# Kernel tuning notes

Hardware: AMD Instinct MI355X
Metric: run time of the kernel (lower is better)

Reference implementation:

```python
import jax, jax.numpy as jnp
import numpy as np

N_NODES = 50000
IN_CH = 128
HID = 128
N_EDGES = 800000


def _glorot(key, shape):
    fan_in, fan_out = shape[0], shape[1]
    lim = (6.0 / (fan_in + fan_out)) ** 0.5
    return jax.random.uniform(key, shape, jnp.float32, -lim, lim)


def setup_inputs() -> dict:
    key = jax.random.key(0)
    ks = jax.random.split(key, 8)
    x = jax.random.normal(ks[0], (N_NODES, IN_CH), jnp.float32)
    edge_index = jax.random.randint(ks[1], (2, N_EDGES), 0, N_NODES, jnp.int64)
    return {
        "x": x,
        "edge_index": edge_index,
        # SAGEConv1: lin_l (with bias) applied to mean-aggregated neighbors,
        # lin_r (no bias) applied to root features (PyG defaults, mean aggr)
        "W1l": _glorot(ks[2], (IN_CH, HID)),
        "b1l": jnp.zeros((HID,), jnp.float32),
        "W1r": _glorot(ks[3], (IN_CH, HID)),
        # SAGEConv2
        "W2l": _glorot(ks[4], (HID, HID)),
        "b2l": jnp.zeros((HID,), jnp.float32),
        "W2r": _glorot(ks[5], (HID, HID)),
        # final Linear(hidden, 1)
        "Wout": _glorot(ks[6], (HID, 1)),
        "bout": jnp.zeros((1,), jnp.float32),
    }


def _sage_conv(x, src, dst, Wl, bl, Wr, n_nodes):
    # gather source features along edges, mean-reduce into destinations
    msgs = x[src]                                                # [E, D]
    sums = jax.ops.segment_sum(msgs, dst, num_segments=n_nodes)  # [N, D]
    cnt = jax.ops.segment_sum(jnp.ones((src.shape[0], 1), x.dtype), dst,
                              num_segments=n_nodes)              # [N, 1]
    agg = sums / jnp.maximum(cnt, 1.0)
    return agg @ Wl + bl + x @ Wr


def reference(x, edge_index, W1l, b1l, W1r, W2l, b2l, W2r, Wout, bout):
    src, dst = edge_index[0], edge_index[1]
    n = x.shape[0]
    h = jax.nn.relu(_sage_conv(x, src, dst, W1l, b1l, W1r, n))
    h = jax.nn.relu(_sage_conv(h, src, dst, W2l, b2l, W2r, n))
    return (h @ Wout + bout).squeeze(-1)  # [N]
```

## Files before the change

kernel.cpp:

```cpp
#include <hip/hip_runtime.h>

#define D 128
#define LSTR 132
#define CAP 3072
#define NBLK 256

typedef __attribute__((ext_vector_type(8))) short short8;
typedef __attribute__((ext_vector_type(4))) float f32x4;

static __device__ __forceinline__ unsigned short f2bf(float f) {
    unsigned u = __float_as_uint(f);
    return (unsigned short)((u + 0x7fffu + ((u >> 16) & 1u)) >> 16);
}
static __device__ __forceinline__ float b2f(unsigned short u) {
    return __uint_as_float(((unsigned)u) << 16);
}


__global__ __launch_bounds__(256) void prep_hist_kernel(
    const float* __restrict__ x, const float* __restrict__ W1l,
    const float* __restrict__ W1r, const float* __restrict__ W2l,
    const float* __restrict__ W2r, unsigned* __restrict__ xb2,
    unsigned short* __restrict__ Bt1, unsigned short* __restrict__ Bt2,
    int NX2, const int* __restrict__ dst, int E, int nbins,
    unsigned* __restrict__ G) {
    const int t = threadIdx.x;
    if (blockIdx.x < NBLK) {
        __shared__ int h[2048];
        for (int i = t; i < nbins; i += 256) h[i] = 0;
        __syncthreads();
        const int per = (E + NBLK - 1) / NBLK;
        const int lo = blockIdx.x * per;
        const int hi = min(lo + per, E);
        for (int i = lo + t; i < hi; i += 256) atomicAdd(&h[dst[i] >> 5], 1);
        __syncthreads();
        for (int i = t; i < nbins; i += 256)
            G[(size_t)i * NBLK + blockIdx.x] = (unsigned)h[i];
        return;
    }
    const int i = (blockIdx.x - NBLK) * 256 + t;
    if (i < NX2) {
        const float2 v = *(const float2*)(x + 2 * (size_t)i);
        xb2[i] = (unsigned)f2bf(v.x) | ((unsigned)f2bf(v.y) << 16);
    } else if (i < NX2 + 2 * 32768) {
        const int j = i - NX2;
        const int which = j >> 15;
        const int jj = j & 32767;
        const int n = jj >> 8;
        const int k = jj & 255;
        const float* Wl = which ? W2l : W1l;
        const float* Wr = which ? W2r : W1r;
        const float w = (k < 128) ? Wl[k * 128 + n] : Wr[(k - 128) * 128 + n];
        (which ? Bt2 : Bt1)[jj] = f2bf(w);
    }
}

__global__ __launch_bounds__(256) void scanB_kernel(unsigned* __restrict__ G,
                                                    int nbins,
                                                    int* __restrict__ tot) {
    const int wave = threadIdx.x >> 6;
    const int lane = threadIdx.x & 63;
    const int bin = blockIdx.x * 4 + wave;
    if (bin >= nbins) return;
    unsigned* p = G + (size_t)bin * NBLK + lane * 4;
    uint4 v = *(uint4*)p;
    const unsigned s = v.x + v.y + v.z + v.w;
    unsigned sc = s;
#pragma unroll
    for (int off = 1; off < 64; off <<= 1) {
        const unsigned u = (unsigned)__shfl_up((int)sc, off, 64);
        if (lane >= off) sc += u;
    }
    const unsigned excl = sc - s;
    uint4 w;
    w.x = excl;
    w.y = excl + v.x;
    w.z = excl + v.x + v.y;
    w.w = excl + v.x + v.y + v.z;
    *(uint4*)p = w;
    if (lane == 63) tot[bin] = (int)(excl + s);
}

__global__ __launch_bounds__(1024) void scanC_kernel(
    const int* __restrict__ tot, int nbins, int* __restrict__ tile_base) {
    __shared__ int part[1024];
    const int t = threadIdx.x;
    const int chunk = (nbins + 1023) >> 10;
    const int lo = min(t * chunk, nbins);
    const int hi = min(lo + chunk, nbins);
    int s = 0;
    for (int i = lo; i < hi; ++i) s += tot[i];
    part[t] = s;
    __syncthreads();
    for (int off = 1; off < 1024; off <<= 1) {
        int add = (t >= off) ? part[t - off] : 0;
        __syncthreads();
        part[t] += add;
        __syncthreads();
    }
    int excl = (t == 0) ? 0 : part[t - 1];
    for (int i = lo; i < hi; ++i) {
        tile_base[i] = excl;
        excl += tot[i];
    }
    if (t == 1023) tile_base[nbins] = part[1023];
}

__global__ __launch_bounds__(256) void fillB_kernel(
    const int* __restrict__ src, const int* __restrict__ dst, int E,
    const unsigned* __restrict__ G, const int* __restrict__ tile_base,
    unsigned* __restrict__ csr, int nbins) {
    __shared__ int rank[2048];
    __shared__ int base[2048];
    const int t = threadIdx.x;
    for (int i = t; i < nbins; i += 256) {
        rank[i] = 0;
        base[i] = tile_base[i] + (int)G[(size_t)i * NBLK + blockIdx.x];
    }
    __syncthreads();
    const int per = (E + NBLK - 1) / NBLK;
    const int lo = blockIdx.x * per;
    const int hi = min(lo + per, E);
    for (int i = lo + t; i < hi; i += 256) {
        const int d = dst[i];
        const int bin = d >> 5;
        const int r = atomicAdd(&rank[bin], 1);
        csr[base[bin] + r] = (unsigned)src[i] | ((unsigned)d << 16);
    }
}

__global__ __launch_bounds__(256) void sortT_kernel(unsigned* __restrict__ csr,
                                                    const int* __restrict__
                                                        tile_base,
                                                    float* __restrict__ invL_g,
                                                    int N) {
    __shared__ unsigned sortedE[CAP];
    __shared__ int rowcnt[32];
    __shared__ int rowofs[32];
    const int b = blockIdx.x;
    const int i0 = b * 32;
    const int t = threadIdx.x;
    const int rs0 = tile_base[b];
    const int re0 = tile_base[b + 1];
    const int nE = re0 - rs0;

    if (t < 32) rowcnt[t] = 0;
    __syncthreads();
    for (int i = t; i < nE; i += 256)
        atomicAdd(&rowcnt[(csr[rs0 + i] >> 16) & 31], 1);
    __syncthreads();
    if (t < 32) {
        const int v = rowcnt[t];
        if (i0 + t < N) invL_g[i0 + t] = 1.0f / fmaxf((float)v, 1.0f);
        int s = v;
#pragma unroll
        for (int off = 1; off < 32; off <<= 1) {
            const int u = __shfl_up(s, off, 32);
            if ((t & 31) >= off) s += u;
        }
        rowofs[t] = s - v;
    }
    __syncthreads();
    if (nE <= CAP) {
        for (int i = t; i < nE; i += 256) {
            const unsigned p = csr[rs0 + i];
            const int k = atomicAdd(&rowofs[(p >> 16) & 31], 1);
            sortedE[k] = p;
        }
        __syncthreads();
        for (int i = t; i < nE; i += 256) csr[rs0 + i] = sortedE[i];
    }
}

template <bool HEAD>
__global__ __launch_bounds__(256) void sage_kernel(
    const unsigned short* __restrict__ xb, const unsigned* __restrict__ csr,
    const int* __restrict__ tile_base, const float* __restrict__ invL_g,
    const unsigned short* __restrict__ Bt,
    const float* __restrict__ bl, const float* __restrict__ Wout,
    const float* __restrict__ bout, unsigned short* __restrict__ hb_out,
    float* __restrict__ out, int N) {
    __shared__ float aggL[32 * LSTR];
    __shared__ float invL[32];
    __shared__ float redH[64];

    const int b = blockIdx.x;
    const int i0 = b * 32;
    const int t = threadIdx.x;
    const int g = t >> 5;
    const int l = t & 31;
    const int c4 = l << 2;

    for (int i = t; i < 32 * LSTR; i += 256) aggL[i] = 0.f;
    if (t < 32) invL[t] = (i0 + t < N) ? invL_g[i0 + t] : 1.0f;
    __syncthreads();

    const int rs0 = tile_base[b];
    const int re0 = tile_base[b + 1];
    const int nE = re0 - rs0;
    int e = rs0 + ((nE * g) >> 3);
    const int ee = rs0 + ((nE * (g + 1)) >> 3);

    float4 acc = make_float4(0.f, 0.f, 0.f, 0.f);
    int cur = (e < ee) ? (int)(csr[e] >> 16) - i0 : -1;

    auto load4 = [&](unsigned p) -> float4 {
        const ushort4 u =
            *(const ushort4*)(xb + (size_t)(p & 0xffffu) * D + c4);
        float4 v;
        v.x = b2f(u.x); v.y = b2f(u.y); v.z = b2f(u.z); v.w = b2f(u.w);
        return v;
    };
    auto step = [&](unsigned p, const float4& v) {
        const int r = (int)(p >> 16) - i0;
        if (r != cur) {
            float* q = aggL + cur * LSTR + c4;
            atomicAdd(q + 0, acc.x);
            atomicAdd(q + 1, acc.y);
            atomicAdd(q + 2, acc.z);
            atomicAdd(q + 3, acc.w);
            acc = make_float4(0.f, 0.f, 0.f, 0.f);
            cur = r;
        }
        acc.x += v.x; acc.y += v.y; acc.z += v.z; acc.w += v.w;
    };

    while (e + 8 <= ee) {
        const unsigned p0 = csr[e + 0], p1 = csr[e + 1];
        const unsigned p2 = csr[e + 2], p3 = csr[e + 3];
        const unsigned p4 = csr[e + 4], p5 = csr[e + 5];
        const unsigned p6 = csr[e + 6], p7 = csr[e + 7];
        const float4 v0 = load4(p0), v1 = load4(p1), v2 = load4(p2),
                     v3 = load4(p3), v4 = load4(p4), v5 = load4(p5),
                     v6 = load4(p6), v7 = load4(p7);
        step(p0, v0); step(p1, v1); step(p2, v2); step(p3, v3);
        step(p4, v4); step(p5, v5); step(p6, v6); step(p7, v7);
        e += 8;
    }
    while (e < ee) {
        const unsigned p = csr[e];
        step(p, load4(p));
        ++e;
    }
    if (cur >= 0) {
        float* q = aggL + cur * LSTR + c4;
        atomicAdd(q + 0, acc.x);
        atomicAdd(q + 1, acc.y);
        atomicAdd(q + 2, acc.z);
        atomicAdd(q + 3, acc.w);
    }
    __syncthreads();

    const int wave = t >> 6;
    const int lane = t & 63;
    const int ln = lane & 15;
    const int quad = lane >> 4;
    const int mtile = wave & 1;
    const int nt0 = (wave >> 1) * 4;
    const int mrow = mtile * 16 + ln;
    const int gmr = i0 + mrow;
    const float inv = invL[mrow];

    f32x4 acc4[4] = {f32x4{0.f, 0.f, 0.f, 0.f}, f32x4{0.f, 0.f, 0.f, 0.f},
                     f32x4{0.f, 0.f, 0.f, 0.f}, f32x4{0.f, 0.f, 0.f, 0.f}};

#pragma unroll
    for (int s = 0; s < 4; ++s) {
        const int kb = s * 32 + quad * 8;
        const float* ap = aggL + mrow * LSTR + kb;
        const float4 fa = *(const float4*)ap;
        const float4 fb = *(const float4*)(ap + 4);
        const short8 aA = {(short)f2bf(fa.x * inv), (short)f2bf(fa.y * inv),
                           (short)f2bf(fa.z * inv), (short)f2bf(fa.w * inv),
                           (short)f2bf(fb.x * inv), (short)f2bf(fb.y * inv),
                           (short)f2bf(fb.z * inv), (short)f2bf(fb.w * inv)};
        short8 aX = {0, 0, 0, 0, 0, 0, 0, 0};
        if (gmr < N) aX = *(const short8*)(xb + (size_t)gmr * D + kb);
#pragma unroll
        for (int nt = 0; nt < 4; ++nt) {
            const int n = (nt0 + nt) * 16 + ln;
            const short8 b1 = *(const short8*)(Bt + n * 256 + kb);
            const short8 b2 = *(const short8*)(Bt + n * 256 + 128 + kb);
            acc4[nt] = __builtin_amdgcn_mfma_f32_16x16x32_bf16(aA, b1, acc4[nt],
                                                               0, 0, 0);
            acc4[nt] = __builtin_amdgcn_mfma_f32_16x16x32_bf16(aX, b2, acc4[nt],
                                                               0, 0, 0);
        }
    }

    float biasv[4], woutv[4];
#pragma unroll
    for (int nt = 0; nt < 4; ++nt) {
        const int col = (nt0 + nt) * 16 + ln;
        biasv[nt] = bl[col];
        if (HEAD) woutv[nt] = Wout[col];
    }

    if (!HEAD) {
#pragma unroll
        for (int r = 0; r < 4; ++r) {
            const int gr = i0 + mtile * 16 + quad * 4 + r;
            if (gr < N) {
#pragma unroll
                for (int nt = 0; nt < 4; ++nt) {
                    const int col = (nt0 + nt) * 16 + ln;
                    const float v = fmaxf(acc4[nt][r] + biasv[nt], 0.f);
                    hb_out[(size_t)gr * D + col] = f2bf(v);
                }
            }
        }
    } else {
        const float b0 = bout[0];
#pragma unroll
        for (int r = 0; r < 4; ++r) {
            const int row = mtile * 16 + quad * 4 + r;
            float p = 0.f;
#pragma unroll
            for (int nt = 0; nt < 4; ++nt) {
                const float v = fmaxf(acc4[nt][r] + biasv[nt], 0.f);
                p += v * woutv[nt];
            }
            p += __shfl_xor(p, 1);
            p += __shfl_xor(p, 2);
            p += __shfl_xor(p, 4);
            p += __shfl_xor(p, 8);
            if (ln == 0) redH[row * 2 + (wave >> 1)] = p;
        }
        __syncthreads();
        if (t < 32) {
            const int gr = i0 + t;
            if (gr < N) out[gr] = redH[t * 2] + redH[t * 2 + 1] + b0;
        }
    }
}

extern "C" void kernel_launch(void* const* d_in, const int* in_sizes, int n_in,
                              void* d_out, int out_size, void* d_ws,
                              size_t ws_size, hipStream_t stream) {
    const float* x = (const float*)d_in[0];
    const int* ei = (const int*)d_in[1];
    const float* W1l = (const float*)d_in[2];
    const float* b1l = (const float*)d_in[3];
    const float* W1r = (const float*)d_in[4];
    const float* W2l = (const float*)d_in[5];
    const float* b2l = (const float*)d_in[6];
    const float* W2r = (const float*)d_in[7];
    const float* Wout = (const float*)d_in[8];
    const float* bout = (const float*)d_in[9];

    const int N = in_sizes[0] / D;
    const int E = in_sizes[1] / 2;
    const int* src = ei;
    const int* dst = ei + E;

    const int nbins = (N + 31) / 32;
    const size_t Npad = (size_t)((N + 255) & ~255);
    const size_t Epad = (size_t)((E + 255) & ~255);

    int* tot = (int*)d_ws;
    int* tile_base = tot + 2048;
    float* invL_g = (float*)(tile_base + 2052);
    unsigned* G = (unsigned*)(invL_g + Npad);
    unsigned* csr = G + (size_t)2048 * NBLK;
    unsigned short* xb = (unsigned short*)(csr + Epad);
    unsigned short* hb = xb + (size_t)N * D;
    unsigned short* Bt1 = hb + (size_t)N * D;
    unsigned short* Bt2 = Bt1 + 128 * 256;
    float* out = (float*)d_out;

    const int NX2 = N * D / 2;
    const int prep_blocks = (NX2 + 2 * 32768 + 255) / 256;

    prep_hist_kernel<<<NBLK + prep_blocks, 256, 0, stream>>>(
        x, W1l, W1r, W2l, W2r, (unsigned*)xb, Bt1, Bt2, NX2, dst, E, nbins, G);
    scanB_kernel<<<(nbins + 3) / 4, 256, 0, stream>>>(G, nbins, tot);
    scanC_kernel<<<1, 1024, 0, stream>>>(tot, nbins, tile_base);
    fillB_kernel<<<NBLK, 256, 0, stream>>>(src, dst, E, G, tile_base, csr,
                                           nbins);
    sortT_kernel<<<nbins, 256, 0, stream>>>(csr, tile_base, invL_g, N);

    sage_kernel<false><<<nbins, 256, 0, stream>>>(
        xb, csr, tile_base, invL_g, Bt1, b1l, nullptr, nullptr, hb, nullptr, N);
    sage_kernel<true><<<nbins, 256, 0, stream>>>(
        hb, csr, tile_base, invL_g, Bt2, b2l, Wout, bout, nullptr, out, N);
}
```

Before: 259.4 us.

## Replace binned two-level CSR build with per-node degree atomics and cursor fill

Drops the per-block bin histogram, two scan passes, binned fill and per-tile local sort. In their place it counts per-node degree with global atomics, runs a single-block scan over all nodes that writes cursors, tile bases and inverse degrees, and fills the CSR with per-destination atomic cursors. This removes two kernel launches and the shared-memory sort. The cost is heavy global atomic contention, a serial scan over 50k nodes in one block, and edges within a row landing in nondeterministic order. The aggregation loop is also rewritten to software-prefetch the next eight CSR entries and unpack bf16 pairs directly, and the launch bounds gain an occupancy hint.

```diff
diff --git a/kernel.cpp b/kernel.cpp
--- a/kernel.cpp
+++ b/kernel.cpp
@@ -2,8 +2,7 @@
 
 #define D 128
 #define LSTR 132
-#define CAP 3072
-#define NBLK 256
+#define HB 256
 
 typedef __attribute__((ext_vector_type(8))) short short8;
 typedef __attribute__((ext_vector_type(4))) float f32x4;
@@ -11,9 +10,6 @@
 static __device__ __forceinline__ unsigned short f2bf(float f) {
     unsigned u = __float_as_uint(f);
     return (unsigned short)((u + 0x7fffu + ((u >> 16) & 1u)) >> 16);
-}
-static __device__ __forceinline__ float b2f(unsigned short u) {
-    return __uint_as_float(((unsigned)u) << 16);
 }
 
 
@@ -22,23 +18,16 @@
     const float* __restrict__ W1r, const float* __restrict__ W2l,
     const float* __restrict__ W2r, unsigned* __restrict__ xb2,
     unsigned short* __restrict__ Bt1, unsigned short* __restrict__ Bt2,
-    int NX2, const int* __restrict__ dst, int E, int nbins,
-    unsigned* __restrict__ G) {
+    int NX2, const int* __restrict__ dst, int E, int* __restrict__ deg) {
     const int t = threadIdx.x;
-    if (blockIdx.x < NBLK) {
-        __shared__ int h[2048];
-        for (int i = t; i < nbins; i += 256) h[i] = 0;
-        __syncthreads();
-        const int per = (E + NBLK - 1) / NBLK;
+    if (blockIdx.x < HB) {
+        const int per = (E + HB - 1) / HB;
         const int lo = blockIdx.x * per;
         const int hi = min(lo + per, E);
-        for (int i = lo + t; i < hi; i += 256) atomicAdd(&h[dst[i] >> 5], 1);
-        __syncthreads();
-        for (int i = t; i < nbins; i += 256)
-            G[(size_t)i * NBLK + blockIdx.x] = (unsigned)h[i];
+        for (int i = lo + t; i < hi; i += 256) atomicAdd(&deg[dst[i]], 1);
         return;
     }
-    const int i = (blockIdx.x - NBLK) * 256 + t;
+    const int i = (blockIdx.x - HB) * 256 + t;
     if (i < NX2) {
         const float2 v = *(const float2*)(x + 2 * (size_t)i);
         xb2[i] = (unsigned)f2bf(v.x) | ((unsigned)f2bf(v.y) << 16);
@@ -55,41 +44,17 @@
     }
 }
 
-__global__ __launch_bounds__(256) void scanB_kernel(unsigned* __restrict__ G,
-                                                    int nbins,
-                                                    int* __restrict__ tot) {
-    const int wave = threadIdx.x >> 6;
-    const int lane = threadIdx.x & 63;
-    const int bin = blockIdx.x * 4 + wave;
-    if (bin >= nbins) return;
-    unsigned* p = G + (size_t)bin * NBLK + lane * 4;
-    uint4 v = *(uint4*)p;
-    const unsigned s = v.x + v.y + v.z + v.w;
-    unsigned sc = s;
-#pragma unroll
-    for (int off = 1; off < 64; off <<= 1) {
-        const unsigned u = (unsigned)__shfl_up((int)sc, off, 64);
-        if (lane >= off) sc += u;
-    }
-    const unsigned excl = sc - s;
-    uint4 w;
-    w.x = excl;
-    w.y = excl + v.x;
-    w.z = excl + v.x + v.y;
-    w.w = excl + v.x + v.y + v.z;
-    *(uint4*)p = w;
-    if (lane == 63) tot[bin] = (int)(excl + s);
-}
-
-__global__ __launch_bounds__(1024) void scanC_kernel(
-    const int* __restrict__ tot, int nbins, int* __restrict__ tile_base) {
+__global__ __launch_bounds__(1024) void scan_kernel(
+    const int* __restrict__ deg, int N, int E, int nbins,
+    int* __restrict__ cursor, int* __restrict__ tile_base,
+    float* __restrict__ invL_g) {
     __shared__ int part[1024];
     const int t = threadIdx.x;
-    const int chunk = (nbins + 1023) >> 10;
-    const int lo = min(t * chunk, nbins);
-    const int hi = min(lo + chunk, nbins);
+    const int chunk = (N + 1023) >> 10;
+    const int lo = min(t * chunk, N);
+    const int hi = min(lo + chunk, N);
     int s = 0;
-    for (int i = lo; i < hi; ++i) s += tot[i];
+    for (int i = lo; i < hi; ++i) s += deg[i];
     part[t] = s;
     __syncthreads();
     for (int off = 1; off < 1024; off <<= 1) {
@@ -98,82 +63,30 @@
         part[t] += add;
         __syncthreads();
     }
-    int excl = (t == 0) ? 0 : part[t - 1];
+    int run = (t == 0) ? 0 : part[t - 1];
     for (int i = lo; i < hi; ++i) {
-        tile_base[i] = excl;
-        excl += tot[i];
-    }
-    if (t == 1023) tile_base[nbins] = part[1023];
-}
-
-__global__ __launch_bounds__(256) void fillB_kernel(
+        cursor[i] = run;
+        if ((i & 31) == 0) tile_base[i >> 5] = run;
+        const int d = deg[i];
+        invL_g[i] = 1.0f / fmaxf((float)d, 1.0f);
+        run += d;
+    }
+    if (t == 0) tile_base[nbins] = E;
+}
+
+__global__ __launch_bounds__(256) void fill_kernel(
     const int* __restrict__ src, const int* __restrict__ dst, int E,
-    const unsigned* __restrict__ G, const int* __restrict__ tile_base,
-    unsigned* __restrict__ csr, int nbins) {
-    __shared__ int rank[2048];
-    __shared__ int base[2048];
-    const int t = threadIdx.x;
-    for (int i = t; i < nbins; i += 256) {
-        rank[i] = 0;
-        base[i] = tile_base[i] + (int)G[(size_t)i * NBLK + blockIdx.x];
-    }
-    __syncthreads();
-    const int per = (E + NBLK - 1) / NBLK;
-    const int lo = blockIdx.x * per;
-    const int hi = min(lo + per, E);
-    for (int i = lo + t; i < hi; i += 256) {
+    int* __restrict__ cursor, unsigned* __restrict__ csr) {
+    const int i = blockIdx.x * 256 + threadIdx.x;
+    if (i < E) {
         const int d = dst[i];
-        const int bin = d >> 5;
-        const int r = atomicAdd(&rank[bin], 1);
-        csr[base[bin] + r] = (unsigned)src[i] | ((unsigned)d << 16);
-    }
-}
-
-__global__ __launch_bounds__(256) void sortT_kernel(unsigned* __restrict__ csr,
-                                                    const int* __restrict__
-                                                        tile_base,
-                                                    float* __restrict__ invL_g,
-                                                    int N) {
-    __shared__ unsigned sortedE[CAP];
-    __shared__ int rowcnt[32];
-    __shared__ int rowofs[32];
-    const int b = blockIdx.x;
-    const int i0 = b * 32;
-    const int t = threadIdx.x;
-    const int rs0 = tile_base[b];
-    const int re0 = tile_base[b + 1];
-    const int nE = re0 - rs0;
-
-    if (t < 32) rowcnt[t] = 0;
-    __syncthreads();
-    for (int i = t; i < nE; i += 256)
-        atomicAdd(&rowcnt[(csr[rs0 + i] >> 16) & 31], 1);
-    __syncthreads();
-    if (t < 32) {
-        const int v = rowcnt[t];
-        if (i0 + t < N) invL_g[i0 + t] = 1.0f / fmaxf((float)v, 1.0f);
-        int s = v;
-#pragma unroll
-        for (int off = 1; off < 32; off <<= 1) {
-            const int u = __shfl_up(s, off, 32);
-            if ((t & 31) >= off) s += u;
-        }
-        rowofs[t] = s - v;
-    }
-    __syncthreads();
-    if (nE <= CAP) {
-        for (int i = t; i < nE; i += 256) {
-            const unsigned p = csr[rs0 + i];
-            const int k = atomicAdd(&rowofs[(p >> 16) & 31], 1);
-            sortedE[k] = p;
-        }
-        __syncthreads();
-        for (int i = t; i < nE; i += 256) csr[rs0 + i] = sortedE[i];
+        const int pos = atomicAdd(&cursor[d], 1);
+        csr[pos] = (unsigned)src[i] | ((unsigned)d << 16);
     }
 }
 
 template <bool HEAD>
-__global__ __launch_bounds__(256) void sage_kernel(
+__global__ __launch_bounds__(256, 4) void sage_kernel(
     const unsigned short* __restrict__ xb, const unsigned* __restrict__ csr,
     const int* __restrict__ tile_base, const float* __restrict__ invL_g,
     const unsigned short* __restrict__ Bt,
@@ -202,53 +115,58 @@
     const int ee = rs0 + ((nE * (g + 1)) >> 3);
 
     float4 acc = make_float4(0.f, 0.f, 0.f, 0.f);
-    int cur = (e < ee) ? (int)(csr[e] >> 16) - i0 : -1;
-
-    auto load4 = [&](unsigned p) -> float4 {
-        const ushort4 u =
-            *(const ushort4*)(xb + (size_t)(p & 0xffffu) * D + c4);
-        float4 v;
-        v.x = b2f(u.x); v.y = b2f(u.y); v.z = b2f(u.z); v.w = b2f(u.w);
-        return v;
-    };
-    auto step = [&](unsigned p, const float4& v) {
-        const int r = (int)(p >> 16) - i0;
-        if (r != cur) {
-            float* q = aggL + cur * LSTR + c4;
-            atomicAdd(q + 0, acc.x);
-            atomicAdd(q + 1, acc.y);
-            atomicAdd(q + 2, acc.z);
-            atomicAdd(q + 3, acc.w);
-            acc = make_float4(0.f, 0.f, 0.f, 0.f);
-            cur = r;
-        }
-        acc.x += v.x; acc.y += v.y; acc.z += v.z; acc.w += v.w;
-    };
-
-    while (e + 8 <= ee) {
-        const unsigned p0 = csr[e + 0], p1 = csr[e + 1];
-        const unsigned p2 = csr[e + 2], p3 = csr[e + 3];
-        const unsigned p4 = csr[e + 4], p5 = csr[e + 5];
-        const unsigned p6 = csr[e + 6], p7 = csr[e + 7];
-        const float4 v0 = load4(p0), v1 = load4(p1), v2 = load4(p2),
-                     v3 = load4(p3), v4 = load4(p4), v5 = load4(p5),
-                     v6 = load4(p6), v7 = load4(p7);
-        step(p0, v0); step(p1, v1); step(p2, v2); step(p3, v3);
-        step(p4, v4); step(p5, v5); step(p6, v6); step(p7, v7);
-        e += 8;
-    }
-    while (e < ee) {
-        const unsigned p = csr[e];
-        step(p, load4(p));
-        ++e;
-    }
-    if (cur >= 0) {
+    int cur = -1;
+
+    auto flush = [&]() {
         float* q = aggL + cur * LSTR + c4;
         atomicAdd(q + 0, acc.x);
         atomicAdd(q + 1, acc.y);
         atomicAdd(q + 2, acc.z);
         atomicAdd(q + 3, acc.w);
-    }
+    };
+    auto step = [&](unsigned p, uint2 u) {
+        const int r = (int)(p >> 16) - i0;
+        if (r != cur) {
+            if (cur >= 0) flush();
+            acc = make_float4(0.f, 0.f, 0.f, 0.f);
+            cur = r;
+        }
+        acc.x += __uint_as_float(u.x << 16);
+        acc.y += __uint_as_float(u.x & 0xffff0000u);
+        acc.z += __uint_as_float(u.y << 16);
+        acc.w += __uint_as_float(u.y & 0xffff0000u);
+    };
+
+    const int nfull = (ee - e) >> 3;
+    unsigned pc[8];
+    if (nfull > 0) {
+#pragma unroll
+        for (int i = 0; i < 8; ++i) pc[i] = csr[e + i];
+    }
+    for (int k = 0; k < nfull; ++k) {
+        uint2 u[8];
+#pragma unroll
+        for (int i = 0; i < 8; ++i)
+            u[i] = *(const uint2*)(xb + (size_t)(pc[i] & 0xffffu) * D + c4);
+        unsigned pf[8];
+        if (k + 1 < nfull) {
+#pragma unroll
+            for (int i = 0; i < 8; ++i) pf[i] = csr[e + 8 + i];
+        }
+#pragma unroll
+        for (int i = 0; i < 8; ++i) step(pc[i], u[i]);
+        if (k + 1 < nfull) {
+#pragma unroll
+            for (int i = 0; i < 8; ++i) pc[i] = pf[i];
+        }
+        e += 8;
+    }
+    for (e = rs0 + ((nE * g) >> 3) + nfull * 8; e < ee; ++e) {
+        const unsigned p = csr[e];
+        const uint2 u = *(const uint2*)(xb + (size_t)(p & 0xffffu) * D + c4);
+        step(p, u);
+    }
+    if (cur >= 0) flush();
     __syncthreads();
 
     const int wave = t >> 6;
@@ -357,11 +275,11 @@
     const size_t Npad = (size_t)((N + 255) & ~255);
     const size_t Epad = (size_t)((E + 255) & ~255);
 
-    int* tot = (int*)d_ws;
-    int* tile_base = tot + 2048;
+    int* deg = (int*)d_ws;
+    int* cursor = deg + Npad;
+    int* tile_base = cursor + Npad;
     float* invL_g = (float*)(tile_base + 2052);
-    unsigned* G = (unsigned*)(invL_g + Npad);
-    unsigned* csr = G + (size_t)2048 * NBLK;
+    unsigned* csr = (unsigned*)(invL_g + Npad);
     unsigned short* xb = (unsigned short*)(csr + Epad);
     unsigned short* hb = xb + (size_t)N * D;
     unsigned short* Bt1 = hb + (size_t)N * D;
@@ -371,13 +289,12 @@
     const int NX2 = N * D / 2;
     const int prep_blocks = (NX2 + 2 * 32768 + 255) / 256;
 
-    prep_hist_kernel<<<NBLK + prep_blocks, 256, 0, stream>>>(
-        x, W1l, W1r, W2l, W2r, (unsigned*)xb, Bt1, Bt2, NX2, dst, E, nbins, G);
-    scanB_kernel<<<(nbins + 3) / 4, 256, 0, stream>>>(G, nbins, tot);
-    scanC_kernel<<<1, 1024, 0, stream>>>(tot, nbins, tile_base);
-    fillB_kernel<<<NBLK, 256, 0, stream>>>(src, dst, E, G, tile_base, csr,
-                                           nbins);
-    sortT_kernel<<<nbins, 256, 0, stream>>>(csr, tile_base, invL_g, N);
+    hipMemsetAsync(deg, 0, Npad * sizeof(int), stream);
+    prep_hist_kernel<<<HB + prep_blocks, 256, 0, stream>>>(
+        x, W1l, W1r, W2l, W2r, (unsigned*)xb, Bt1, Bt2, NX2, dst, E, deg);
+    scan_kernel<<<1, 1024, 0, stream>>>(deg, N, E, nbins, cursor, tile_base,
+                                        invL_g);
+    fill_kernel<<<(E + 255) / 256, 256, 0, stream>>>(src, dst, E, cursor, csr);
 
     sage_kernel<false><<<nbins, 256, 0, stream>>>(
         xb, csr, tile_base, invL_g, Bt1, b1l, nullptr, nullptr, hb, nullptr, N);
```

Measured after the change: 409.0 us. +57.6%, slower.

## Software-pipeline edge gather with 16-byte row loads and four edges per wave

Applied to the files above, without the earlier changes.

Restructures the aggregation phase of the SAGE kernel. Each wave now walks a quarter of the tile's edges with four edge streams per wave, and each lane loads eight bf16 features with one 16-byte load. The next batch of eight edges (indices and feature rows) is prefetched while the current batch is accumulated. The prep kernel converts x to bf16 four elements per thread, and the SAGE kernel gets a launch-bounds occupancy hint. The aim is to hide gather latency and cut load instruction count, at the cost of more registers and more LDS atomics per flush (eight floats per lane).

```diff
diff --git a/kernel.cpp b/kernel.cpp
--- a/kernel.cpp
+++ b/kernel.cpp
@@ -12,17 +12,14 @@
     unsigned u = __float_as_uint(f);
     return (unsigned short)((u + 0x7fffu + ((u >> 16) & 1u)) >> 16);
 }
-static __device__ __forceinline__ float b2f(unsigned short u) {
-    return __uint_as_float(((unsigned)u) << 16);
-}
 
 
 __global__ __launch_bounds__(256) void prep_hist_kernel(
     const float* __restrict__ x, const float* __restrict__ W1l,
     const float* __restrict__ W1r, const float* __restrict__ W2l,
-    const float* __restrict__ W2r, unsigned* __restrict__ xb2,
+    const float* __restrict__ W2r, uint2* __restrict__ xb4,
     unsigned short* __restrict__ Bt1, unsigned short* __restrict__ Bt2,
-    int NX2, const int* __restrict__ dst, int E, int nbins,
+    int NX4, const int* __restrict__ dst, int E, int nbins,
     unsigned* __restrict__ G) {
     const int t = threadIdx.x;
     if (blockIdx.x < NBLK) {
@@ -39,11 +36,14 @@
         return;
     }
     const int i = (blockIdx.x - NBLK) * 256 + t;
-    if (i < NX2) {
-        const float2 v = *(const float2*)(x + 2 * (size_t)i);
-        xb2[i] = (unsigned)f2bf(v.x) | ((unsigned)f2bf(v.y) << 16);
-    } else if (i < NX2 + 2 * 32768) {
-        const int j = i - NX2;
+    if (i < NX4) {
+        const float4 v = *(const float4*)(x + 4 * (size_t)i);
+        uint2 o;
+        o.x = (unsigned)f2bf(v.x) | ((unsigned)f2bf(v.y) << 16);
+        o.y = (unsigned)f2bf(v.z) | ((unsigned)f2bf(v.w) << 16);
+        xb4[i] = o;
+    } else if (i < NX4 + 2 * 32768) {
+        const int j = i - NX4;
         const int which = j >> 15;
         const int jj = j & 32767;
         const int n = jj >> 8;
@@ -173,7 +173,7 @@
 }
 
 template <bool HEAD>
-__global__ __launch_bounds__(256) void sage_kernel(
+__global__ __launch_bounds__(256, 2) void sage_kernel(
     const unsigned short* __restrict__ xb, const unsigned* __restrict__ csr,
     const int* __restrict__ tile_base, const float* __restrict__ invL_g,
     const unsigned short* __restrict__ Bt,
@@ -187,9 +187,11 @@
     const int b = blockIdx.x;
     const int i0 = b * 32;
     const int t = threadIdx.x;
-    const int g = t >> 5;
-    const int l = t & 31;
-    const int c4 = l << 2;
+    const int wv = t >> 6;
+    const int lane = t & 63;
+    const int sub = lane >> 4;
+    const int cl = lane & 15;
+    const int c8 = cl << 3;
 
     for (int i = t; i < 32 * LSTR; i += 256) aggL[i] = 0.f;
     if (t < 32) invL[t] = (i0 + t < N) ? invL_g[i0 + t] : 1.0f;
@@ -198,65 +200,88 @@
     const int rs0 = tile_base[b];
     const int re0 = tile_base[b + 1];
     const int nE = re0 - rs0;
-    int e = rs0 + ((nE * g) >> 3);
-    const int ee = rs0 + ((nE * (g + 1)) >> 3);
-
-    float4 acc = make_float4(0.f, 0.f, 0.f, 0.f);
-    int cur = (e < ee) ? (int)(csr[e] >> 16) - i0 : -1;
-
-    auto load4 = [&](unsigned p) -> float4 {
-        const ushort4 u =
-            *(const ushort4*)(xb + (size_t)(p & 0xffffu) * D + c4);
-        float4 v;
-        v.x = b2f(u.x); v.y = b2f(u.y); v.z = b2f(u.z); v.w = b2f(u.w);
-        return v;
-    };
-    auto step = [&](unsigned p, const float4& v) {
-        const int r = (int)(p >> 16) - i0;
-        if (r != cur) {
-            float* q = aggL + cur * LSTR + c4;
-            atomicAdd(q + 0, acc.x);
-            atomicAdd(q + 1, acc.y);
-            atomicAdd(q + 2, acc.z);
-            atomicAdd(q + 3, acc.w);
-            acc = make_float4(0.f, 0.f, 0.f, 0.f);
-            cur = r;
-        }
-        acc.x += v.x; acc.y += v.y; acc.z += v.z; acc.w += v.w;
-    };
-
-    while (e + 8 <= ee) {
-        const unsigned p0 = csr[e + 0], p1 = csr[e + 1];
-        const unsigned p2 = csr[e + 2], p3 = csr[e + 3];
-        const unsigned p4 = csr[e + 4], p5 = csr[e + 5];
-        const unsigned p6 = csr[e + 6], p7 = csr[e + 7];
-        const float4 v0 = load4(p0), v1 = load4(p1), v2 = load4(p2),
-                     v3 = load4(p3), v4 = load4(p4), v5 = load4(p5),
-                     v6 = load4(p6), v7 = load4(p7);
-        step(p0, v0); step(p1, v1); step(p2, v2); step(p3, v3);
-        step(p4, v4); step(p5, v5); step(p6, v6); step(p7, v7);
-        e += 8;
-    }
-    while (e < ee) {
-        const unsigned p = csr[e];
-        step(p, load4(p));
-        ++e;
-    }
-    if (cur >= 0) {
-        float* q = aggL + cur * LSTR + c4;
-        atomicAdd(q + 0, acc.x);
-        atomicAdd(q + 1, acc.y);
-        atomicAdd(q + 2, acc.z);
-        atomicAdd(q + 3, acc.w);
-    }
-    __syncthreads();
-
-    const int wave = t >> 6;
-    const int lane = t & 63;
+    const int ws_ = rs0 + ((nE * wv) >> 2);
+    const int we_ = rs0 + ((nE * (wv + 1)) >> 2);
+    const int cnt = we_ - ws_;
+    const int lastc = re0 - 1;
+
+    float a[8];
+#pragma unroll
+    for (int j = 0; j < 8; ++j) a[j] = 0.f;
+    int cur = -1;
+
+    if (cnt > 0) {
+        const int nb = (cnt + 31) >> 5;
+        unsigned dc[8];
+        uint4 vc[8];
+        {
+            const int e0 = ws_ + sub;
+#pragma unroll
+            for (int j = 0; j < 8; ++j) dc[j] = csr[min(e0 + 4 * j, lastc)];
+#pragma unroll
+            for (int j = 0; j < 8; ++j)
+                vc[j] =
+                    *(const uint4*)(xb + (size_t)(dc[j] & 0xffffu) * D + c8);
+        }
+        for (int k = 0; k < nb; ++k) {
+            unsigned dn[8];
+            uint4 vn[8];
+            const bool more = (k + 1 < nb);
+            if (more) {
+                const int e1 = ws_ + (k + 1) * 32 + sub;
+#pragma unroll
+                for (int j = 0; j < 8; ++j) dn[j] = csr[min(e1 + 4 * j, lastc)];
+#pragma unroll
+                for (int j = 0; j < 8; ++j)
+                    vn[j] = *(const uint4*)(xb +
+                                            (size_t)(dn[j] & 0xffffu) * D + c8);
+            }
+            const int e0 = ws_ + k * 32 + sub;
+#pragma unroll
+            for (int j = 0; j < 8; ++j) {
+                if (e0 + 4 * j < we_) {
+                    const int r = (int)(dc[j] >> 16) - i0;
+                    if (r != cur) {
+                        if (cur >= 0) {
+                            float* q = aggL + cur * LSTR + c8;
+#pragma unroll
+                            for (int m = 0; m < 8; ++m) atomicAdd(q + m, a[m]);
+#pragma unroll
+                            for (int m = 0; m < 8; ++m) a[m] = 0.f;
+                        }
+                        cur = r;
+                    }
+                    const uint4 u = vc[j];
+                    a[0] += __uint_as_float(u.x << 16);
+                    a[1] += __uint_as_float(u.x & 0xffff0000u);
+                    a[2] += __uint_as_float(u.y << 16);
+                    a[3] += __uint_as_float(u.y & 0xffff0000u);
+                    a[4] += __uint_as_float(u.z << 16);
+                    a[5] += __uint_as_float(u.z & 0xffff0000u);
+                    a[6] += __uint_as_float(u.w << 16);
+                    a[7] += __uint_as_float(u.w & 0xffff0000u);
+                }
+            }
+            if (more) {
+#pragma unroll
+                for (int j = 0; j < 8; ++j) {
+                    dc[j] = dn[j];
+                    vc[j] = vn[j];
+                }
+            }
+        }
+        if (cur >= 0) {
+            float* q = aggL + cur * LSTR + c8;
+#pragma unroll
+            for (int m = 0; m < 8; ++m) atomicAdd(q + m, a[m]);
+        }
+    }
+    __syncthreads();
+
     const int ln = lane & 15;
     const int quad = lane >> 4;
-    const int mtile = wave & 1;
-    const int nt0 = (wave >> 1) * 4;
+    const int mtile = wv & 1;
+    const int nt0 = (wv >> 1) * 4;
     const int mrow = mtile * 16 + ln;
     const int gmr = i0 + mrow;
     const float inv = invL[mrow];
@@ -324,7 +349,7 @@
             p += __shfl_xor(p, 2);
             p += __shfl_xor(p, 4);
             p += __shfl_xor(p, 8);
-            if (ln == 0) redH[row * 2 + (wave >> 1)] = p;
+            if (ln == 0) redH[row * 2 + (wv >> 1)] = p;
         }
         __syncthreads();
         if (t < 32) {
@@ -368,11 +393,11 @@
     unsigned short* Bt2 = Bt1 + 128 * 256;
     float* out = (float*)d_out;
 
-    const int NX2 = N * D / 2;
-    const int prep_blocks = (NX2 + 2 * 32768 + 255) / 256;
+    const int NX4 = N * D / 4;
+    const int prep_blocks = (NX4 + 2 * 32768 + 255) / 256;
 
     prep_hist_kernel<<<NBLK + prep_blocks, 256, 0, stream>>>(
-        x, W1l, W1r, W2l, W2r, (unsigned*)xb, Bt1, Bt2, NX2, dst, E, nbins, G);
+        x, W1l, W1r, W2l, W2r, (uint2*)xb, Bt1, Bt2, NX4, dst, E, nbins, G);
     scanB_kernel<<<(nbins + 3) / 4, 256, 0, stream>>>(G, nbins, tot);
     scanC_kernel<<<1, 1024, 0, stream>>>(tot, nbins, tile_base);
     fillB_kernel<<<NBLK, 256, 0, stream>>>(src, dst, E, G, tile_base, csr,
```

Measured after the change: 465.2 us. 1.79x slower.

## Slice bf16 features by column blocks and split layer-1 aggregation into sliced gather kernel

Applied to the files above, without the earlier changes.

Stores bf16 node features in a column-sliced layout of eight 16-column slices, so each gathered row segment is a contiguous 32-byte chunk. Layer 1 is split into a gather kernel, launched once per tile per slice, that accumulates into a global fp32 agg buffer, and a separate MFMA GEMM kernel that reads it back. Each slice's gather then touches a smaller working set, which should improve cache locality on random neighbour reads. The cost is an extra fp32 round trip through global memory for agg, plus one more kernel launch.

```diff
diff --git a/kernel.cpp b/kernel.cpp
--- a/kernel.cpp
+++ b/kernel.cpp
@@ -4,6 +4,7 @@
 #define LSTR 132
 #define CAP 3072
 #define NBLK 256
+#define NSL 8
 
 typedef __attribute__((ext_vector_type(8))) short short8;
 typedef __attribute__((ext_vector_type(4))) float f32x4;
@@ -20,9 +21,9 @@
 __global__ __launch_bounds__(256) void prep_hist_kernel(
     const float* __restrict__ x, const float* __restrict__ W1l,
     const float* __restrict__ W1r, const float* __restrict__ W2l,
-    const float* __restrict__ W2r, unsigned* __restrict__ xb2,
+    const float* __restrict__ W2r, unsigned short* __restrict__ xbS,
     unsigned short* __restrict__ Bt1, unsigned short* __restrict__ Bt2,
-    int NX2, const int* __restrict__ dst, int E, int nbins,
+    int NC, int N, const int* __restrict__ dst, int E, int nbins,
     unsigned* __restrict__ G) {
     const int t = threadIdx.x;
     if (blockIdx.x < NBLK) {
@@ -39,11 +40,28 @@
         return;
     }
     const int i = (blockIdx.x - NBLK) * 256 + t;
-    if (i < NX2) {
-        const float2 v = *(const float2*)(x + 2 * (size_t)i);
-        xb2[i] = (unsigned)f2bf(v.x) | ((unsigned)f2bf(v.y) << 16);
-    } else if (i < NX2 + 2 * 32768) {
-        const int j = i - NX2;
+    if (i < NC) {
+        const int s = i / N;
+        const int v = i - s * N;
+        const float* xp = x + (size_t)v * 128 + s * 16;
+        const float4 f0 = *(const float4*)(xp + 0);
+        const float4 f1 = *(const float4*)(xp + 4);
+        const float4 f2 = *(const float4*)(xp + 8);
+        const float4 f3 = *(const float4*)(xp + 12);
+        uint4 lo, hi;
+        lo.x = (unsigned)f2bf(f0.x) | ((unsigned)f2bf(f0.y) << 16);
+        lo.y = (unsigned)f2bf(f0.z) | ((unsigned)f2bf(f0.w) << 16);
+        lo.z = (unsigned)f2bf(f1.x) | ((unsigned)f2bf(f1.y) << 16);
+        lo.w = (unsigned)f2bf(f1.z) | ((unsigned)f2bf(f1.w) << 16);
+        hi.x = (unsigned)f2bf(f2.x) | ((unsigned)f2bf(f2.y) << 16);
+        hi.y = (unsigned)f2bf(f2.z) | ((unsigned)f2bf(f2.w) << 16);
+        hi.z = (unsigned)f2bf(f3.x) | ((unsigned)f2bf(f3.y) << 16);
+        hi.w = (unsigned)f2bf(f3.z) | ((unsigned)f2bf(f3.w) << 16);
+        unsigned short* op = xbS + ((size_t)s * N + v) * 16;
+        *(uint4*)op = lo;
+        *(uint4*)(op + 8) = hi;
+    } else if (i < NC + 2 * 32768) {
+        const int j = i - NC;
         const int which = j >> 15;
         const int jj = j & 32767;
         const int n = jj >> 8;
@@ -172,6 +190,154 @@
     }
 }
 
+__global__ __launch_bounds__(256) void sageA_kernel(
+    const unsigned short* __restrict__ xbS, const unsigned* __restrict__ csr,
+    const int* __restrict__ tile_base, float* __restrict__ agg, int N) {
+    __shared__ float aggS[32][16];
+    const int bid = blockIdx.x;
+    const int s = bid & 7;
+    const int b = bid >> 3;
+    const int i0 = b * 32;
+    const int t = threadIdx.x;
+
+    if (t < 128) ((f32x4*)&aggS[0][0])[t] = f32x4{0.f, 0.f, 0.f, 0.f};
+    __syncthreads();
+
+    const int rs0 = tile_base[b];
+    const int re0 = tile_base[b + 1];
+    const int nE = re0 - rs0;
+    const int wv = t >> 6;
+    const int lane = t & 63;
+    const int k = lane >> 1;
+    const int h = lane & 1;
+    const int we0 = rs0 + ((nE * wv) >> 2);
+    const int wcnt = (rs0 + ((nE * (wv + 1)) >> 2)) - we0;
+    int e = we0 + ((wcnt * k) >> 5);
+    const int pe = we0 + ((wcnt * (k + 1)) >> 5);
+
+    const unsigned short* base = xbS + (size_t)s * N * 16 + h * 8;
+
+    float a[8];
+#pragma unroll
+    for (int m = 0; m < 8; ++m) a[m] = 0.f;
+    int cur = -1;
+
+    auto ld = [&](unsigned p) -> uint4 {
+        return *(const uint4*)(base + (size_t)(p & 0xffffu) * 16);
+    };
+    auto flush = [&]() {
+        float* q = &aggS[cur][h * 8];
+#pragma unroll
+        for (int m = 0; m < 8; ++m) atomicAdd(q + m, a[m]);
+    };
+    auto step = [&](unsigned p, const uint4& u) {
+        const int r = (int)(p >> 16) - i0;
+        if (r != cur) {
+            if (cur >= 0) flush();
+#pragma unroll
+            for (int m = 0; m < 8; ++m) a[m] = 0.f;
+            cur = r;
+        }
+        a[0] += __uint_as_float(u.x << 16);
+        a[1] += __uint_as_float(u.x & 0xffff0000u);
+        a[2] += __uint_as_float(u.y << 16);
+        a[3] += __uint_as_float(u.y & 0xffff0000u);
+        a[4] += __uint_as_float(u.z << 16);
+        a[5] += __uint_as_float(u.z & 0xffff0000u);
+        a[6] += __uint_as_float(u.w << 16);
+        a[7] += __uint_as_float(u.w & 0xffff0000u);
+    };
+
+    while (e + 4 <= pe) {
+        const unsigned p0 = __builtin_nontemporal_load(csr + e + 0);
+        const unsigned p1 = __builtin_nontemporal_load(csr + e + 1);
+        const unsigned p2 = __builtin_nontemporal_load(csr + e + 2);
+        const unsigned p3 = __builtin_nontemporal_load(csr + e + 3);
+        const uint4 u0 = ld(p0), u1 = ld(p1), u2 = ld(p2), u3 = ld(p3);
+        step(p0, u0);
+        step(p1, u1);
+        step(p2, u2);
+        step(p3, u3);
+        e += 4;
+    }
+    while (e < pe) {
+        const unsigned p = __builtin_nontemporal_load(csr + e);
+        step(p, ld(p));
+        ++e;
+    }
+    if (cur >= 0) flush();
+    __syncthreads();
+
+    const int row = t >> 3;
+    const int c2 = (t & 7) * 2;
+    float* dp = agg + (size_t)(i0 + row) * 128 + s * 16 + c2;
+    __builtin_nontemporal_store(aggS[row][c2], dp);
+    __builtin_nontemporal_store(aggS[row][c2 + 1], dp + 1);
+}
+
+__global__ __launch_bounds__(256) void sageB_kernel(
+    const float* __restrict__ agg, const unsigned short* __restrict__ xbS,
+    const float* __restrict__ invL_g, const unsigned short* __restrict__ Bt,
+    const float* __restrict__ bl, unsigned short* __restrict__ hbS, int N) {
+    const int b = blockIdx.x;
+    const int i0 = b * 32;
+    const int t = threadIdx.x;
+    const int wave = t >> 6;
+    const int lane = t & 63;
+    const int ln = lane & 15;
+    const int quad = lane >> 4;
+    const int mtile = wave & 1;
+    const int nt0 = (wave >> 1) * 4;
+    const int mrow = mtile * 16 + ln;
+    const int gmr = i0 + mrow;
+    const float inv = (gmr < N) ? invL_g[gmr] : 1.0f;
+
+    f32x4 acc4[4] = {f32x4{0.f, 0.f, 0.f, 0.f}, f32x4{0.f, 0.f, 0.f, 0.f},
+                     f32x4{0.f, 0.f, 0.f, 0.f}, f32x4{0.f, 0.f, 0.f, 0.f}};
+
+#pragma unroll
+    for (int s4 = 0; s4 < 4; ++s4) {
+        const int kb = s4 * 32 + quad * 8;
+        const float* ap = agg + (size_t)gmr * 128 + kb;
+        const float4 fa = *(const float4*)ap;
+        const float4 fb = *(const float4*)(ap + 4);
+        const short8 aA = {(short)f2bf(fa.x * inv), (short)f2bf(fa.y * inv),
+                           (short)f2bf(fa.z * inv), (short)f2bf(fa.w * inv),
+                           (short)f2bf(fb.x * inv), (short)f2bf(fb.y * inv),
+                           (short)f2bf(fb.z * inv), (short)f2bf(fb.w * inv)};
+        short8 aX = {0, 0, 0, 0, 0, 0, 0, 0};
+        if (gmr < N)
+            aX = *(const short8*)(xbS + ((size_t)(kb >> 4) * N + gmr) * 16 +
+                                  (kb & 15));
+#pragma unroll
+        for (int nt = 0; nt < 4; ++nt) {
+            const int n = (nt0 + nt) * 16 + ln;
+            const short8 b1 = *(const short8*)(Bt + n * 256 + kb);
+            const short8 b2 = *(const short8*)(Bt + n * 256 + 128 + kb);
+            acc4[nt] = __builtin_amdgcn_mfma_f32_16x16x32_bf16(aA, b1, acc4[nt],
+                                                               0, 0, 0);
+            acc4[nt] = __builtin_amdgcn_mfma_f32_16x16x32_bf16(aX, b2, acc4[nt],
+                                                               0, 0, 0);
+        }
+    }
+
+    float biasv[4];
+#pragma unroll
+    for (int nt = 0; nt < 4; ++nt) biasv[nt] = bl[(nt0 + nt) * 16 + ln];
+
+#pragma unroll
+    for (int r = 0; r < 4; ++r) {
+        const int gr = i0 + mtile * 16 + quad * 4 + r;
+        if (gr < N) {
+#pragma unroll
+            for (int nt = 0; nt < 4; ++nt) {
+                const float v = fmaxf(acc4[nt][r] + biasv[nt], 0.f);
+                hbS[((size_t)(nt0 + nt) * N + gr) * 16 + ln] = f2bf(v);
+            }
+        }
+    }
+}
+
 template <bool HEAD>
 __global__ __launch_bounds__(256) void sage_kernel(
     const unsigned short* __restrict__ xb, const unsigned* __restrict__ csr,
@@ -201,12 +367,13 @@
     int e = rs0 + ((nE * g) >> 3);
     const int ee = rs0 + ((nE * (g + 1)) >> 3);
 
+    const unsigned short* gbase = xb + (size_t)(l >> 2) * N * 16 + (l & 3) * 4;
+
     float4 acc = make_float4(0.f, 0.f, 0.f, 0.f);
     int cur = (e < ee) ? (int)(csr[e] >> 16) - i0 : -1;
 
     auto load4 = [&](unsigned p) -> float4 {
-        const ushort4 u =
-            *(const ushort4*)(xb + (size_t)(p & 0xffffu) * D + c4);
+        const ushort4 u = *(const ushort4*)(gbase + (size_t)(p & 0xffffu) * 16);
         float4 v;
         v.x = b2f(u.x); v.y = b2f(u.y); v.z = b2f(u.z); v.w = b2f(u.w);
         return v;
@@ -265,8 +432,8 @@
                      f32x4{0.f, 0.f, 0.f, 0.f}, f32x4{0.f, 0.f, 0.f, 0.f}};
 
 #pragma unroll
-    for (int s = 0; s < 4; ++s) {
-        const int kb = s * 32 + quad * 8;
+    for (int s4 = 0; s4 < 4; ++s4) {
+        const int kb = s4 * 32 + quad * 8;
         const float* ap = aggL + mrow * LSTR + kb;
         const float4 fa = *(const float4*)ap;
         const float4 fb = *(const float4*)(ap + 4);
@@ -275,7 +442,9 @@
                            (short)f2bf(fb.x * inv), (short)f2bf(fb.y * inv),
                            (short)f2bf(fb.z * inv), (short)f2bf(fb.w * inv)};
         short8 aX = {0, 0, 0, 0, 0, 0, 0, 0};
-        if (gmr < N) aX = *(const short8*)(xb + (size_t)gmr * D + kb);
+        if (gmr < N)
+            aX = *(const short8*)(xb + ((size_t)(kb >> 4) * N + gmr) * 16 +
+                                  (kb & 15));
 #pragma unroll
         for (int nt = 0; nt < 4; ++nt) {
             const int n = (nt0 + nt) * 16 + ln;
@@ -303,9 +472,8 @@
             if (gr < N) {
 #pragma unroll
                 for (int nt = 0; nt < 4; ++nt) {
-                    const int col = (nt0 + nt) * 16 + ln;
                     const float v = fmaxf(acc4[nt][r] + biasv[nt], 0.f);
-                    hb_out[(size_t)gr * D + col] = f2bf(v);
+                    hb_out[((size_t)(nt0 + nt) * N + gr) * 16 + ln] = f2bf(v);
                 }
             }
         }
@@ -362,25 +530,26 @@
     float* invL_g = (float*)(tile_base + 2052);
     unsigned* G = (unsigned*)(invL_g + Npad);
     unsigned* csr = G + (size_t)2048 * NBLK;
-    unsigned short* xb = (unsigned short*)(csr + Epad);
-    unsigned short* hb = xb + (size_t)N * D;
-    unsigned short* Bt1 = hb + (size_t)N * D;
+    float* agg = (float*)(csr + Epad);
+    unsigned short* xbS = (unsigned short*)(agg + Npad * 128);
+    unsigned short* hbS = xbS + (size_t)N * D;
+    unsigned short* Bt1 = hbS + (size_t)N * D;
     unsigned short* Bt2 = Bt1 + 128 * 256;
     float* out = (float*)d_out;
 
-    const int NX2 = N * D / 2;
-    const int prep_blocks = (NX2 + 2 * 32768 + 255) / 256;
+    const int NC = N * NSL;
+    const int prep_blocks = (NC + 2 * 32768 + 255) / 256;
 
     prep_hist_kernel<<<NBLK + prep_blocks, 256, 0, stream>>>(
-        x, W1l, W1r, W2l, W2r, (unsigned*)xb, Bt1, Bt2, NX2, dst, E, nbins, G);
+        x, W1l, W1r, W2l, W2r, xbS, Bt1, Bt2, NC, N, dst, E, nbins, G);
     scanB_kernel<<<(nbins + 3) / 4, 256, 0, stream>>>(G, nbins, tot);
     scanC_kernel<<<1, 1024, 0, stream>>>(tot, nbins, tile_base);
     fillB_kernel<<<NBLK, 256, 0, stream>>>(src, dst, E, G, tile_base, csr,
                                            nbins);
     sortT_kernel<<<nbins, 256, 0, stream>>>(csr, tile_base, invL_g, N);
 
-    sage_kernel<false><<<nbins, 256, 0, stream>>>(
-        xb, csr, tile_base, invL_g, Bt1, b1l, nullptr, nullptr, hb, nullptr, N);
+    sageA_kernel<<<nbins * NSL, 256, 0, stream>>>(xbS, csr, tile_base, agg, N);
+    sageB_kernel<<<nbins, 256, 0, stream>>>(agg, xbS, invL_g, Bt1, b1l, hbS, N);
     sage_kernel<true><<<nbins, 256, 0, stream>>>(
-        hb, csr, tile_base, invL_g, Bt2, b2l, Wout, bout, nullptr, out, N);
-}
+        hbS, csr, tile_base, invL_g, Bt2, b2l, Wout, bout, nullptr, out, N);
+}
```

Result: slower. 444.4 us (+71.3%).
